# Kernel optimization log

Hardware: AMD Instinct MI355X
Metric: run time of the kernel (lower is better)

Reference implementation:

```python
import jax, jax.numpy as jnp
import numpy as np

B = 524288          # batch size
C = 64              # continuous dims
D = 8               # categorical dims
NCAT = 6            # categories per dim -> 6**8 = 1679616 total
NB = 21             # ceil(log2(6**8)) binary dims


def setup_inputs() -> dict:
    key = jax.random.key(0)
    k1, k2, k3 = jax.random.split(key, 3)
    inputs_continuous = jax.random.normal(k1, (B, C), dtype=jnp.float32)
    inputs_categorical = jax.random.randint(k2, (B, D), 0, NCAT, dtype=jnp.int32)
    # uniform dequantization noise in (0,1); keep away from 0 so log() is finite
    dequantization_noise = jax.random.uniform(k3, (B, 2 * NB), dtype=jnp.float32,
                                              minval=0.01, maxval=1.0)
    num_per_dim = jnp.full((D,), NCAT, dtype=jnp.int32)
    # category_factors[i] = prod(num_per_dim[:i]) (mixed-radix factors)
    category_factors = jnp.concatenate(
        [jnp.ones((1,), jnp.int32), jnp.cumprod(num_per_dim[:-1])]).astype(jnp.int32)
    binary_mask = (2 ** jnp.arange(NB - 1, -1, -1)).astype(jnp.int32)
    return {
        "inputs_continuous": inputs_continuous,
        "inputs_categorical": inputs_categorical,
        "dequantization_noise": dequantization_noise,
        "category_factors": category_factors,
        "binary_mask": binary_mask,
    }


def reference(inputs_continuous, inputs_categorical, dequantization_noise,
              category_factors, binary_mask):
    b = inputs_categorical.shape[0]
    nb = binary_mask.shape[0]
    # mixed-radix encode categories to a single decimal code: [B]
    decimal_encoded = jnp.sum(category_factors * inputs_categorical, axis=-1)
    # binary encode: [B, nb] bool
    binary_encoded = (decimal_encoded[:, None] & binary_mask) != 0
    # View noise as [B, nb, 2]; torch code gathers/scatters flat indices
    # 2i + (0 if bit else 1) for max slot, 2i + (1 if bit else 0) for min slot.
    view = dequantization_noise.reshape(b, nb, 2)
    v0, v1 = view[..., 0], view[..., 1]
    max_v = jnp.where(binary_encoded, v0, v1)
    min_v = jnp.where(binary_encoded, v1, v0)
    rescaling_log_probs = -jnp.sum(jnp.log(max_v), axis=-1)  # [B]
    new_min = min_v * max_v  # scatter-multiply into the min slots
    n0 = jnp.where(binary_encoded, max_v, new_min)
    n1 = jnp.where(binary_encoded, new_min, max_v)
    noise_out = jnp.stack([n0, n1], axis=-1).reshape(b, 2 * nb)
    out_continuous = jnp.concatenate([inputs_continuous, noise_out], axis=1)
    # uniform dequantizer: log prob of U(0,1) samples is 0
    dequantization_log_probs = jnp.zeros((b,), out_continuous.dtype)
    return out_continuous, dequantization_log_probs - rescaling_log_probs
```

## Files before the change

kernel.cpp:

```cpp
#include <hip/hip_runtime.h>


constexpr int NB = 21;
constexpr int OUT_COLS = 106;
constexpr int ROWS_PER_BLOCK = 16;

__global__ __launch_bounds__(256) void dequant_fused_kernel(
    const float* __restrict__ cont,
    const int*   __restrict__ cat,
    const float* __restrict__ noise,
    float* __restrict__ out,
    int B)
{
    const int tid  = threadIdx.x;
    const int wave = tid >> 6;
    const int lane = tid & 63;
    const int half = lane >> 5;
    const int l    = lane & 31;
    const int g0   = blockIdx.x * ROWS_PER_BLOCK + wave * 4;

    const int  crow = g0 + (lane >> 4);
    const int  cc   = lane & 15;
    const bool cok  = crow < B;
    float4 cv = make_float4(0.f, 0.f, 0.f, 0.f);
    if (cok) cv = *reinterpret_cast<const float4*>(cont + (size_t)crow * 64 + 4 * cc);

    const int  nrow0 = g0 + half;
    const int  nrow1 = g0 + 2 + half;
    const bool nok0  = nrow0 < B;
    const bool nok1  = nrow1 < B;
    float2 nv0 = make_float2(1.f, 1.f), nv1 = make_float2(1.f, 1.f);
    if (l < NB) {
        if (nok0) nv0 = *reinterpret_cast<const float2*>(noise + (size_t)nrow0 * 42 + 2 * l);
        if (nok1) nv1 = *reinterpret_cast<const float2*>(noise + (size_t)nrow1 * 42 + 2 * l);
    }

    int dec0 = 0, dec1 = 0;
    if (nok0) {
        const int4 a = *reinterpret_cast<const int4*>(cat + (size_t)nrow0 * 8);
        const int4 b = *reinterpret_cast<const int4*>(cat + (size_t)nrow0 * 8 + 4);
        dec0 = ((((((b.w * 6 + b.z) * 6 + b.y) * 6 + b.x) * 6 + a.w) * 6 + a.z) * 6 + a.y) * 6 + a.x;
    }
    if (nok1) {
        const int4 a = *reinterpret_cast<const int4*>(cat + (size_t)nrow1 * 8);
        const int4 b = *reinterpret_cast<const int4*>(cat + (size_t)nrow1 * 8 + 4);
        dec1 = ((((((b.w * 6 + b.z) * 6 + b.y) * 6 + b.x) * 6 + a.w) * 6 + a.z) * 6 + a.y) * 6 + a.x;
    }

    {
        float lg = 0.f;
        if (nok0 && l < NB) {
            const int   bit  = (dec0 >> (20 - l)) & 1;
            const float maxv = bit ? nv0.x : nv0.y;
            const float minv = bit ? nv0.y : nv0.x;
            lg = __logf(maxv);
            const float nm = minv * maxv;
            float2 o;
            o.x = bit ? maxv : nm;
            o.y = bit ? nm : maxv;
            *reinterpret_cast<float2*>(out + (size_t)nrow0 * OUT_COLS + 64 + 2 * l) = o;
        }
        float s = lg;
#pragma unroll
        for (int m = 16; m; m >>= 1) s += __shfl_xor(s, m, 32);
        if (nok0 && l == 0) out[(size_t)B * OUT_COLS + nrow0] = s;
    }
    {
        float lg = 0.f;
        if (nok1 && l < NB) {
            const int   bit  = (dec1 >> (20 - l)) & 1;
            const float maxv = bit ? nv1.x : nv1.y;
            const float minv = bit ? nv1.y : nv1.x;
            lg = __logf(maxv);
            const float nm = minv * maxv;
            float2 o;
            o.x = bit ? maxv : nm;
            o.y = bit ? nm : maxv;
            *reinterpret_cast<float2*>(out + (size_t)nrow1 * OUT_COLS + 64 + 2 * l) = o;
        }
        float s = lg;
#pragma unroll
        for (int m = 16; m; m >>= 1) s += __shfl_xor(s, m, 32);
        if (nok1 && l == 0) out[(size_t)B * OUT_COLS + nrow1] = s;
    }

    if (cok) {
        float* op = out + (size_t)crow * OUT_COLS + 4 * cc;
        *reinterpret_cast<float2*>(op)     = make_float2(cv.x, cv.y);
        *reinterpret_cast<float2*>(op + 2) = make_float2(cv.z, cv.w);
    }
}

extern "C" void kernel_launch(void* const* d_in, const int* in_sizes, int n_in,
                              void* d_out, int out_size, void* d_ws, size_t ws_size,
                              hipStream_t stream) {
    const float* cont  = (const float*)d_in[0];
    const int*   cat   = (const int*)d_in[1];
    const float* noise = (const float*)d_in[2];

    float* out = (float*)d_out;
    const int B = in_sizes[1] / 8;

    const int grid = (B + ROWS_PER_BLOCK - 1) / ROWS_PER_BLOCK;
    dequant_fused_kernel<<<grid, 256, 0, stream>>>(cont, cat, noise, out, B);
}
```

Measured before the change: 97.95 us.

## Stage row pairs in LDS to emit contiguous float4 output stores

Each wave now handles four pairs of rows. Every pair is assembled into a 212-float contiguous region in shared memory (continuous values plus transformed noise), then written to global memory as 53 aligned float4 stores per pair. The old kernel wrote float2 pieces scattered by row. The goal is better-coalesced, wider stores to the 106-column output, whose row stride is only 8-byte aligned. The cost is an LDS round trip per pair, 32 rows per block instead of 16, and the loss of the tail guard on the second row of each pair, which assumes B is even.

```diff
diff --git a/kernel.cpp b/kernel.cpp
--- a/kernel.cpp
+++ b/kernel.cpp
@@ -3,7 +3,10 @@
 
 constexpr int NB = 21;
 constexpr int OUT_COLS = 106;
-constexpr int ROWS_PER_BLOCK = 16;
+constexpr int PAIR_STRIDE = 216;
+constexpr int PAIRS_PER_WAVE = 4;
+constexpr int WAVES = 4;
+constexpr int ROWS_PER_BLOCK = WAVES * PAIRS_PER_WAVE * 2;
 
 __global__ __launch_bounds__(256) void dequant_fused_kernel(
     const float* __restrict__ cont,
@@ -12,82 +15,61 @@
     float* __restrict__ out,
     int B)
 {
+    __shared__ float sbuf[WAVES * PAIRS_PER_WAVE * PAIR_STRIDE];
+
     const int tid  = threadIdx.x;
     const int wave = tid >> 6;
     const int lane = tid & 63;
     const int half = lane >> 5;
     const int l    = lane & 31;
-    const int g0   = blockIdx.x * ROWS_PER_BLOCK + wave * 4;
 
-    const int  crow = g0 + (lane >> 4);
-    const int  cc   = lane & 15;
-    const bool cok  = crow < B;
-    float4 cv = make_float4(0.f, 0.f, 0.f, 0.f);
-    if (cok) cv = *reinterpret_cast<const float4*>(cont + (size_t)crow * 64 + 4 * cc);
+    const int wrow0 = blockIdx.x * ROWS_PER_BLOCK + wave * (PAIRS_PER_WAVE * 2);
 
-    const int  nrow0 = g0 + half;
-    const int  nrow1 = g0 + 2 + half;
-    const bool nok0  = nrow0 < B;
-    const bool nok1  = nrow1 < B;
-    float2 nv0 = make_float2(1.f, 1.f), nv1 = make_float2(1.f, 1.f);
-    if (l < NB) {
-        if (nok0) nv0 = *reinterpret_cast<const float2*>(noise + (size_t)nrow0 * 42 + 2 * l);
-        if (nok1) nv1 = *reinterpret_cast<const float2*>(noise + (size_t)nrow1 * 42 + 2 * l);
-    }
+#pragma unroll
+    for (int p = 0; p < PAIRS_PER_WAVE; ++p) {
+        const int ra = wrow0 + 2 * p;
+        if (ra >= B) break;
+        float* buf = sbuf + (wave * PAIRS_PER_WAVE + p) * PAIR_STRIDE;
 
-    int dec0 = 0, dec1 = 0;
-    if (nok0) {
-        const int4 a = *reinterpret_cast<const int4*>(cat + (size_t)nrow0 * 8);
-        const int4 b = *reinterpret_cast<const int4*>(cat + (size_t)nrow0 * 8 + 4);
-        dec0 = ((((((b.w * 6 + b.z) * 6 + b.y) * 6 + b.x) * 6 + a.w) * 6 + a.z) * 6 + a.y) * 6 + a.x;
-    }
-    if (nok1) {
-        const int4 a = *reinterpret_cast<const int4*>(cat + (size_t)nrow1 * 8);
-        const int4 b = *reinterpret_cast<const int4*>(cat + (size_t)nrow1 * 8 + 4);
-        dec1 = ((((((b.w * 6 + b.z) * 6 + b.y) * 6 + b.x) * 6 + a.w) * 6 + a.z) * 6 + a.y) * 6 + a.x;
-    }
+        const int c = 2 * lane;
+        const float2 cv =
+            *reinterpret_cast<const float2*>(cont + (size_t)ra * 64 + c);
 
-    {
+        const int nrow = ra + half;
+        float2 nv = make_float2(1.f, 1.f);
+        if (l < NB)
+            nv = *reinterpret_cast<const float2*>(noise + (size_t)nrow * 42 + 2 * l);
+
+        const int4 a  = *reinterpret_cast<const int4*>(cat + (size_t)nrow * 8);
+        const int4 bq = *reinterpret_cast<const int4*>(cat + (size_t)nrow * 8 + 4);
+        const int dec = ((((((bq.w * 6 + bq.z) * 6 + bq.y) * 6 + bq.x) * 6
+                           + a.w) * 6 + a.z) * 6 + a.y) * 6 + a.x;
+
         float lg = 0.f;
-        if (nok0 && l < NB) {
-            const int   bit  = (dec0 >> (20 - l)) & 1;
-            const float maxv = bit ? nv0.x : nv0.y;
-            const float minv = bit ? nv0.y : nv0.x;
+        float2 o = make_float2(0.f, 0.f);
+        if (l < NB) {
+            const int   bit  = (dec >> (20 - l)) & 1;
+            const float maxv = bit ? nv.x : nv.y;
+            const float minv = bit ? nv.y : nv.x;
             lg = __logf(maxv);
             const float nm = minv * maxv;
-            float2 o;
             o.x = bit ? maxv : nm;
             o.y = bit ? nm : maxv;
-            *reinterpret_cast<float2*>(out + (size_t)nrow0 * OUT_COLS + 64 + 2 * l) = o;
         }
+
+        *reinterpret_cast<float2*>(buf + (c < 64 ? c : c + 42)) = cv;
+        if (l < NB)
+            *reinterpret_cast<float2*>(buf + (half ? 170 : 64) + 2 * l) = o;
+
         float s = lg;
 #pragma unroll
         for (int m = 16; m; m >>= 1) s += __shfl_xor(s, m, 32);
-        if (nok0 && l == 0) out[(size_t)B * OUT_COLS + nrow0] = s;
-    }
-    {
-        float lg = 0.f;
-        if (nok1 && l < NB) {
-            const int   bit  = (dec1 >> (20 - l)) & 1;
-            const float maxv = bit ? nv1.x : nv1.y;
-            const float minv = bit ? nv1.y : nv1.x;
-            lg = __logf(maxv);
-            const float nm = minv * maxv;
-            float2 o;
-            o.x = bit ? maxv : nm;
-            o.y = bit ? nm : maxv;
-            *reinterpret_cast<float2*>(out + (size_t)nrow1 * OUT_COLS + 64 + 2 * l) = o;
+        if (l == 0) out[(size_t)B * OUT_COLS + nrow] = s;
+
+        if (lane < 53) {
+            const float4 v = *reinterpret_cast<const float4*>(buf + 4 * lane);
+            *reinterpret_cast<float4*>(out + (size_t)ra * OUT_COLS + 4 * lane) = v;
         }
-        float s = lg;
-#pragma unroll
-        for (int m = 16; m; m >>= 1) s += __shfl_xor(s, m, 32);
-        if (nok1 && l == 0) out[(size_t)B * OUT_COLS + nrow1] = s;
-    }
-
-    if (cok) {
-        float* op = out + (size_t)crow * OUT_COLS + 4 * cc;
-        *reinterpret_cast<float2*>(op)     = make_float2(cv.x, cv.y);
-        *reinterpret_cast<float2*>(op + 2) = make_float2(cv.z, cv.w);
     }
 }
 
```

Measured after the change: 93.76 us. 1.04x faster.
